# Performance work log

Hardware: AMD Instinct MI355X
Metric: run time of the kernel (lower is better)

Reference implementation:

```python
import jax, jax.numpy as jnp
import numpy as np


def _rpad(x):
    # reflect-pad by 1 on both sides along the last dim (matches torch helper)
    return jnp.concatenate([x[..., 1:2], x, x[..., -2:-1]], axis=-1)


def _fwd1d(x):
    # LeGall 5/3 forward lifting along the last dim
    even = x[..., 0::2]
    odd = x[..., 1::2]
    e = _rpad(even)
    pred = 0.5 * (e[..., :-2] + e[..., 2:])
    d = odd - pred                      # detail
    de = _rpad(d)
    upd = 0.25 * (de[..., :-2] + de[..., 2:])
    s = even + upd                      # approx
    return s, d


def setup_inputs() -> dict:
    key = jax.random.key(0)
    # (B, C, H, W) with even H, W so the odd-size reflect pad branch is inactive
    x = jax.random.normal(key, (8, 3, 1024, 1024), dtype=jnp.float32)
    return {"x": x}


def reference(x):
    # rows: transform along W (last dim)
    s_row, d_row = _fwd1d(x)
    # columns: transform along H by swapping H<->W, lifting, swapping back
    LL, LH = _fwd1d(jnp.swapaxes(s_row, 2, 3))
    HL, HH = _fwd1d(jnp.swapaxes(d_row, 2, 3))
    LL, LH, HL, HH = (jnp.swapaxes(t, 2, 3) for t in (LL, LH, HL, HH))
    # (B, 4C, H/2, W/2) subband order [LL, LH, HL, HH]
    return jnp.concatenate([LL, LH, HL, HH], axis=1)
```

## Files before the change

### kernel.cpp

```cpp
#include <hip/hip_runtime.h>


static __device__ __forceinline__ int mref(int k) {
    if (k < 0) return 1;
    if (k > 511) return 510;
    return k;
}

__global__ __launch_bounds__(256) void ilwt53_fused(const float* __restrict__ x,
                                                    float* __restrict__ out) {
    const int tid = threadIdx.x;
    const int c0  = blockIdx.x * 32;
    const int r0  = blockIdx.y * 32;
    const int img = blockIdx.z;

    const int cb = 2 * c0 - 4;
    const int rb = 2 * r0 - 4;

    __shared__ float xt[72 * 73];
    __shared__ float db[72 * 35];
    __shared__ float sb[72 * 33];

    const float* __restrict__ xim = x + (size_t)img * (1024 * 1024);

    #pragma unroll
    for (int n = 0; n < 21; ++n) {
        int i = tid + n * 256;
        if (i < 72 * 72) {
            int lr = i / 72, lc = i - lr * 72;
            int gy = rb + lr; gy = gy < 0 ? 0 : (gy > 1023 ? 1023 : gy);
            int gx = cb + lc; gx = gx < 0 ? 0 : (gx > 1023 ? 1023 : gx);
            xt[lr * 73 + lc] = xim[(size_t)gy * 1024 + gx];
        }
    }
    __syncthreads();

    for (int n = 0; n < 10; ++n) {
        int i = tid + n * 256;
        if (i < 72 * 34) {
            int lr = i / 34, j = i - lr * 34;
            int c = c0 - 1 + j;
            int km1 = mref(c - 1), kp1 = mref(c + 1);
            const float* row = xt + lr * 73;
            float o  = row[2 * (c - c0) + 5];
            float em = row[2 * (km1 - c0) + 4];
            float ep = row[2 * (kp1 - c0) + 4];
            db[lr * 35 + j] = o - 0.5f * (em + ep);
        }
    }
    __syncthreads();

    #pragma unroll
    for (int n = 0; n < 9; ++n) {
        int i = tid + n * 256;
        int lr = i / 32, jj = i & 31;
        int c = c0 + jj;
        int km1 = mref(c - 1), kp1 = mref(c + 1);
        float e  = xt[lr * 73 + 2 * jj + 4];
        float dm = db[lr * 35 + (km1 - c0 + 1)];
        float dp = db[lr * 35 + (kp1 - c0 + 1)];
        sb[lr * 33 + jj] = e + 0.25f * (dm + dp);
    }
    __syncthreads();

    const size_t plane = 512 * 512;
    float* __restrict__ ob = out + ((size_t)(img / 3) * 12 + (img % 3)) * plane;

    #pragma unroll
    for (int p = 0; p < 4; ++p) {
        int i  = tid + p * 256;
        int rr = i >> 5, cc = i & 31;
        int r = r0 + rr, c = c0 + cc;

        const float* sc = sb + cc;
        const float* dc = db + cc + 1;

        auto SE = [&](int k) { return sc[(2 * (k - r0) + 4) * 33]; };
        auto SO = [&](int k) { return sc[(2 * (k - r0) + 5) * 33]; };
        auto DE = [&](int k) { return dc[(2 * (k - r0) + 4) * 35]; };
        auto DO = [&](int k) { return dc[(2 * (k - r0) + 5) * 35]; };

        auto LHf = [&](int k) { return SO(k) - 0.5f * (SE(mref(k - 1)) + SE(mref(k + 1))); };
        auto HHf = [&](int k) { return DO(k) - 0.5f * (DE(mref(k - 1)) + DE(mref(k + 1))); };

        int km = mref(r - 1), kp = mref(r + 1);

        float lh = LHf(r);
        float ll = SE(r) + 0.25f * (LHf(km) + LHf(kp));
        float hh = HHf(r);
        float hl = DE(r) + 0.25f * (HHf(km) + HHf(kp));

        size_t o = (size_t)r * 512 + c;
        ob[o]             = ll;
        ob[o + 3 * plane] = lh;
        ob[o + 6 * plane] = hl;
        ob[o + 9 * plane] = hh;
    }
}

extern "C" void kernel_launch(void* const* d_in, const int* in_sizes, int n_in,
                              void* d_out, int out_size, void* d_ws, size_t ws_size,
                              hipStream_t stream) {
    const float* x = (const float*)d_in[0];
    float* out = (float*)d_out;
    dim3 grid(16, 16, 24);
    dim3 block(256);
    hipLaunchKernelGGL(ilwt53_fused, grid, block, 0, stream, x, out);
}
```

Before: 193.3 us.

## Compute row lifting in registers from float4 loads, vectorize LDS and stores

Each thread now loads a 24-float strip of an input row with float4 global loads and does the horizontal lifting in registers, handling the boundary reflection inline. This drops the raw input tile from shared memory and one sync stage. The column lifting is split into an LH/HH pass followed by an LL/HL pass, both on float4 LDS reads, and the outputs are written as float4. It aims to cut scalar global loads, redundant column recomputation and shared-memory traffic, at the cost of overlapping halo reads and more registers per thread.

```diff
diff --git a/kernel.cpp b/kernel.cpp
--- a/kernel.cpp
+++ b/kernel.cpp
@@ -2,99 +2,137 @@
 
 
 static __device__ __forceinline__ int mref(int k) {
-    if (k < 0) return 1;
-    if (k > 511) return 510;
-    return k;
+    return k < 0 ? 1 : (k > 511 ? 510 : k);
 }
 
-__global__ __launch_bounds__(256) void ilwt53_fused(const float* __restrict__ x,
-                                                    float* __restrict__ out) {
+__global__ __launch_bounds__(256) void ilwt53_v2(const float* __restrict__ x,
+                                                 float* __restrict__ out) {
     const int tid = threadIdx.x;
     const int c0  = blockIdx.x * 32;
     const int r0  = blockIdx.y * 32;
     const int img = blockIdx.z;
+    const int rb  = 2 * r0 - 4;
 
-    const int cb = 2 * c0 - 4;
-    const int rb = 2 * r0 - 4;
-
-    __shared__ float xt[72 * 73];
-    __shared__ float db[72 * 35];
-    __shared__ float sb[72 * 33];
+    __shared__ float sS[72 * 36];
+    __shared__ float sD[72 * 36];
+    __shared__ float sLH[34 * 36];
+    __shared__ float sHH[34 * 36];
 
     const float* __restrict__ xim = x + (size_t)img * (1024 * 1024);
 
     #pragma unroll
-    for (int n = 0; n < 21; ++n) {
-        int i = tid + n * 256;
-        if (i < 72 * 72) {
-            int lr = i / 72, lc = i - lr * 72;
+    for (int it = 0; it < 2; ++it) {
+        int i = tid + it * 256;
+        if (i < 288) {
+            int lr = i >> 2, g = i & 3;
             int gy = rb + lr; gy = gy < 0 ? 0 : (gy > 1023 ? 1023 : gy);
-            int gx = cb + lc; gx = gx < 0 ? 0 : (gx > 1023 ? 1023 : gx);
-            xt[lr * 73 + lc] = xim[(size_t)gy * 1024 + gx];
-        }
-    }
-    __syncthreads();
+            const float* __restrict__ row = xim + (size_t)gy * 1024;
+            int c  = c0 + 8 * g;
+            int fb = 2 * c - 4;
 
-    for (int n = 0; n < 10; ++n) {
-        int i = tid + n * 256;
-        if (i < 72 * 34) {
-            int lr = i / 34, j = i - lr * 34;
-            int c = c0 - 1 + j;
-            int km1 = mref(c - 1), kp1 = mref(c + 1);
-            const float* row = xt + lr * 73;
-            float o  = row[2 * (c - c0) + 5];
-            float em = row[2 * (km1 - c0) + 4];
-            float ep = row[2 * (kp1 - c0) + 4];
-            db[lr * 35 + j] = o - 0.5f * (em + ep);
+            float w[24];
+            if (fb >= 0 && fb + 23 <= 1023) {
+                const float4* p = (const float4*)(row + fb);
+                #pragma unroll
+                for (int q = 0; q < 6; ++q) {
+                    float4 v = p[q];
+                    w[4*q] = v.x; w[4*q+1] = v.y; w[4*q+2] = v.z; w[4*q+3] = v.w;
+                }
+            } else {
+                #pragma unroll
+                for (int q = 0; q < 24; ++q) {
+                    int gx = fb + q; gx = gx < 0 ? 0 : (gx > 1023 ? 1023 : gx);
+                    w[q] = row[gx];
+                }
+            }
+            float d[10];
+            #pragma unroll
+            for (int t = 0; t < 10; ++t)
+                d[t] = w[2*t+3] - 0.5f * (w[2*t] + w[2*t+4]);
+            if (c == 0)   d[1] = w[5]  - w[6];
+            if (c == 504) d[8] = w[19] - w[16];
+
+            float s[8];
+            #pragma unroll
+            for (int i2 = 0; i2 < 8; ++i2)
+                s[i2] = w[2*i2+4] + 0.25f * (d[i2] + d[i2+2]);
+            if (c == 0)   s[0] = w[4]  + 0.5f * d[2];
+            if (c == 504) s[7] = w[18] + 0.5f * d[7];
+
+            float4* ps = (float4*)(sS + lr * 36 + 8 * g);
+            ps[0] = make_float4(s[0], s[1], s[2], s[3]);
+            ps[1] = make_float4(s[4], s[5], s[6], s[7]);
+            float4* pd = (float4*)(sD + lr * 36 + 8 * g);
+            pd[0] = make_float4(d[1], d[2], d[3], d[4]);
+            pd[1] = make_float4(d[5], d[6], d[7], d[8]);
         }
     }
     __syncthreads();
 
     #pragma unroll
-    for (int n = 0; n < 9; ++n) {
-        int i = tid + n * 256;
-        int lr = i / 32, jj = i & 31;
-        int c = c0 + jj;
-        int km1 = mref(c - 1), kp1 = mref(c + 1);
-        float e  = xt[lr * 73 + 2 * jj + 4];
-        float dm = db[lr * 35 + (km1 - c0 + 1)];
-        float dp = db[lr * 35 + (kp1 - c0 + 1)];
-        sb[lr * 33 + jj] = e + 0.25f * (dm + dp);
+    for (int it = 0; it < 2; ++it) {
+        int i = tid + it * 256;
+        if (i < 272) {
+            int j = i >> 3, ccg = i & 7;
+            int k  = r0 - 1 + j;
+            int km = mref(k - 1), kp = mref(k + 1);
+            int lo = 2 * (k  - r0) + 5;
+            int lm = 2 * (km - r0) + 4;
+            int lp = 2 * (kp - r0) + 4;
+            int co = 4 * ccg;
+            float4 so  = *(const float4*)(sS + lo * 36 + co);
+            float4 sem = *(const float4*)(sS + lm * 36 + co);
+            float4 sep = *(const float4*)(sS + lp * 36 + co);
+            float4 dv  = *(const float4*)(sD + lo * 36 + co);
+            float4 dem = *(const float4*)(sD + lm * 36 + co);
+            float4 dep = *(const float4*)(sD + lp * 36 + co);
+            float4 lh, hh;
+            lh.x = so.x - 0.5f * (sem.x + sep.x);
+            lh.y = so.y - 0.5f * (sem.y + sep.y);
+            lh.z = so.z - 0.5f * (sem.z + sep.z);
+            lh.w = so.w - 0.5f * (sem.w + sep.w);
+            hh.x = dv.x - 0.5f * (dem.x + dep.x);
+            hh.y = dv.y - 0.5f * (dem.y + dep.y);
+            hh.z = dv.z - 0.5f * (dem.z + dep.z);
+            hh.w = dv.w - 0.5f * (dem.w + dep.w);
+            *(float4*)(sLH + j * 36 + co) = lh;
+            *(float4*)(sHH + j * 36 + co) = hh;
+        }
     }
     __syncthreads();
 
-    const size_t plane = 512 * 512;
-    float* __restrict__ ob = out + ((size_t)(img / 3) * 12 + (img % 3)) * plane;
+    {
+        int rr = tid >> 3, ccg = tid & 7;
+        int r  = r0 + rr;
+        int km = mref(r - 1), kp = mref(r + 1);
+        int jm = km - (r0 - 1), jc = rr + 1, jp = kp - (r0 - 1);
+        int le = 2 * rr + 4;
+        int co = 4 * ccg;
+        float4 se  = *(const float4*)(sS  + le * 36 + co);
+        float4 de  = *(const float4*)(sD  + le * 36 + co);
+        float4 lhm = *(const float4*)(sLH + jm * 36 + co);
+        float4 lhc = *(const float4*)(sLH + jc * 36 + co);
+        float4 lhp = *(const float4*)(sLH + jp * 36 + co);
+        float4 hhm = *(const float4*)(sHH + jm * 36 + co);
+        float4 hhc = *(const float4*)(sHH + jc * 36 + co);
+        float4 hhp = *(const float4*)(sHH + jp * 36 + co);
+        float4 ll, hl;
+        ll.x = se.x + 0.25f * (lhm.x + lhp.x);
+        ll.y = se.y + 0.25f * (lhm.y + lhp.y);
+        ll.z = se.z + 0.25f * (lhm.z + lhp.z);
+        ll.w = se.w + 0.25f * (lhm.w + lhp.w);
+        hl.x = de.x + 0.25f * (hhm.x + hhp.x);
+        hl.y = de.y + 0.25f * (hhm.y + hhp.y);
+        hl.z = de.z + 0.25f * (hhm.z + hhp.z);
+        hl.w = de.w + 0.25f * (hhm.w + hhp.w);
 
-    #pragma unroll
-    for (int p = 0; p < 4; ++p) {
-        int i  = tid + p * 256;
-        int rr = i >> 5, cc = i & 31;
-        int r = r0 + rr, c = c0 + cc;
-
-        const float* sc = sb + cc;
-        const float* dc = db + cc + 1;
-
-        auto SE = [&](int k) { return sc[(2 * (k - r0) + 4) * 33]; };
-        auto SO = [&](int k) { return sc[(2 * (k - r0) + 5) * 33]; };
-        auto DE = [&](int k) { return dc[(2 * (k - r0) + 4) * 35]; };
-        auto DO = [&](int k) { return dc[(2 * (k - r0) + 5) * 35]; };
-
-        auto LHf = [&](int k) { return SO(k) - 0.5f * (SE(mref(k - 1)) + SE(mref(k + 1))); };
-        auto HHf = [&](int k) { return DO(k) - 0.5f * (DE(mref(k - 1)) + DE(mref(k + 1))); };
-
-        int km = mref(r - 1), kp = mref(r + 1);
-
-        float lh = LHf(r);
-        float ll = SE(r) + 0.25f * (LHf(km) + LHf(kp));
-        float hh = HHf(r);
-        float hl = DE(r) + 0.25f * (HHf(km) + HHf(kp));
-
-        size_t o = (size_t)r * 512 + c;
-        ob[o]             = ll;
-        ob[o + 3 * plane] = lh;
-        ob[o + 6 * plane] = hl;
-        ob[o + 9 * plane] = hh;
+        const size_t plane = 512 * 512;
+        float* __restrict__ ob = out + ((size_t)(img / 3) * 12 + (img % 3)) * plane;
+        size_t o = (size_t)r * 512 + c0 + co;
+        *(float4*)(ob + o)             = ll;
+        *(float4*)(ob + o + 3 * plane) = lhc;
+        *(float4*)(ob + o + 6 * plane) = hl;
+        *(float4*)(ob + o + 9 * plane) = hhc;
     }
 }
 
@@ -105,5 +143,5 @@
     float* out = (float*)d_out;
     dim3 grid(16, 16, 24);
     dim3 block(256);
-    hipLaunchKernelGGL(ilwt53_fused, grid, block, 0, stream, x, out);
+    hipLaunchKernelGGL(ilwt53_v2, grid, block, 0, stream, x, out);
 }
```

New measurement: 177.3 us. 8.3% less time.
